# Kernel optimization log

Measured on AMD Instinct MI355X. Metric: run time of the kernel, lower is better.

## Reference

```python
import jax, jax.numpy as jnp
import numpy as np

BN = 128  # weight block rows
BK = 128  # quantization block along K
FP8_MAX = 448.0  # float8_e4m3fn max finite value
F8 = jnp.float8_e4m3fn


def _quant_dequant_act(x):
    # Dynamic per-token, per-128-block FP8 quantization (scale = amax/448), then dequant.
    M, K = x.shape
    xb = x.reshape(M, K // BK, BK)
    amax = jnp.max(jnp.abs(xb), axis=-1, keepdims=True)
    scale = jnp.maximum(amax, 1e-12) / FP8_MAX
    q = jnp.clip(xb / scale, -FP8_MAX, FP8_MAX).astype(F8)
    return (q.astype(jnp.float32) * scale).reshape(M, K)


def _dequant_weight(w, s):
    # w: (N, K) fp8, s: (N//BN, K//BK) f32 block scales
    N, K = w.shape
    sf = jnp.repeat(jnp.repeat(s, BN, axis=0), BK, axis=1)[:N, :K]
    return w.astype(jnp.float32) * sf


def _fp8_linear(x, w, s):
    # y = dequant(quant(x)) @ dequant(w)^T  -- matches w8a8_fp8_matmul semantics
    return _quant_dequant_act(x) @ _dequant_weight(w, s).T


def _quantize_weight(key, shape):
    E, N, K = shape
    w = jax.random.normal(key, shape, jnp.float32) * 0.02
    wb = w.reshape(E, N // BN, BN, K // BK, BK)
    amax = jnp.max(jnp.abs(wb), axis=(2, 4), keepdims=True)
    scale = jnp.maximum(amax, 1e-12) / FP8_MAX
    q = jnp.clip(wb / scale, -FP8_MAX, FP8_MAX).astype(F8).reshape(E, N, K)
    return q, scale.reshape(E, N // BN, K // BK)


def setup_inputs() -> dict:
    key = jax.random.key(0)
    k1, k2, k3, k4, k5 = jax.random.split(key, 5)
    T, H, I, E, TOPK = 2048, 2048, 1408, 8, 2
    hidden_states = jax.random.normal(k1, (T, H), jnp.float32)
    top_k_index = jax.random.randint(k2, (T, TOPK), 0, E).astype(jnp.int64)
    w = jax.random.uniform(k3, (T, TOPK), jnp.float32)
    top_k_weights = w / jnp.sum(w, axis=-1, keepdims=True)
    gate_up_proj, gate_up_proj_scale_inv = _quantize_weight(k4, (E, 2 * I, H))
    down_proj, down_proj_scale_inv = _quantize_weight(k5, (E, H, I))
    return {
        "hidden_states": hidden_states,
        "top_k_index": top_k_index,
        "top_k_weights": top_k_weights,
        "gate_up_proj": gate_up_proj,
        "gate_up_proj_scale_inv": gate_up_proj_scale_inv,
        "down_proj": down_proj,
        "down_proj_scale_inv": down_proj_scale_inv,
    }


def reference(hidden_states, top_k_index, top_k_weights, gate_up_proj,
              gate_up_proj_scale_inv, down_proj, down_proj_scale_inv):
    E = gate_up_proj.shape[0]
    I = down_proj.shape[-1]
    # Activation quantization is per-token: identical for every expert, compute once.
    x_dq = _quant_dequant_act(hidden_states)  # (T, H)
    out = jnp.zeros_like(hidden_states, dtype=jnp.float32)
    for e in range(E):  # fixed small expert loop (structural, not data dim)
        gu = x_dq @ _dequant_weight(gate_up_proj[e], gate_up_proj_scale_inv[e]).T  # (T, 2I)
        gate, up = gu[:, :I], gu[:, I:]
        h = jax.nn.silu(gate) * up
        d = _fp8_linear(h, down_proj[e], down_proj_scale_inv[e])  # (T, H)
        # routing weight for this expert per token (sums duplicates like index_add_)
        rw = jnp.sum(jnp.where(top_k_index == e, top_k_weights, 0.0), axis=-1)  # (T,)
        out = out + rw[:, None] * d
    return out.astype(hidden_states.dtype)
```

## Files before the change

kernel.cpp:

```cpp
#include <hip/hip_runtime.h>
#include <cstdint>
#include <cstddef>

using f32x4 = __attribute__((ext_vector_type(4))) float;

#define TDIM 2048
#define HDIM 2048
#define IDIM 1408
#define NEXP 8
#define NKB1 16
#define NNB1 11
#define NKB2 11
#define MAXM 4096

__device__ __forceinline__ void gll16(const void* g, void* l) {
  __builtin_amdgcn_global_load_lds(
      (__attribute__((address_space(1))) void*)(uintptr_t)g,
      (__attribute__((address_space(3))) void*)(uint32_t)(uintptr_t)l,
      16, 0, 0);
}

__device__ __forceinline__ f32x4 mfma_fp8(long a, long b, f32x4 c) {
  return __builtin_amdgcn_mfma_f32_16x16x32_fp8_fp8(a, b, c, 0, 0, 0);
}

__device__ __forceinline__ uint32_t f8_1(float q) {
  q = fminf(fmaxf(q, -448.f), 448.f);
  return (uint32_t)__builtin_amdgcn_cvt_pk_fp8_f32(q, q, 0, false) & 0xffu;
}

__device__ __forceinline__ float bf16_to_f32(uint32_t bits16) {
  union { uint32_t u; float f; } c;
  c.u = bits16 << 16;
  return c.f;
}

__global__ void sniff_kernel(const uint16_t* __restrict__ a,
                             const uint16_t* __restrict__ b,
                             int* __restrict__ modes, int* __restrict__ cnt) {
  if (threadIdx.x < 8) cnt[threadIdx.x] = 0;
  if (threadIdx.x == 0) {
    unsigned acc = 0;
    for (int i = 0; i < 128; ++i) acc |= a[2 * i];
    modes[0] = (acc == 0) ? 1 : 0;
    acc = 0;
    for (int i = 0; i < 128; ++i) acc |= b[2 * i];
    modes[1] = (acc == 0) ? 1 : 0;
  }
}

__global__ void repack_kernel(const void* __restrict__ in, uint8_t* __restrict__ out,
                              int n8, const int* __restrict__ modes, int midx) {
  const int i = blockIdx.x * 256 + threadIdx.x;
  if (i >= n8) return;
  const int m = modes[midx];
  float f[8];
  if (m == 1) {
    const float4* p = (const float4*)in;
    float4 a = p[2 * i], b = p[2 * i + 1];
    f[0] = a.x; f[1] = a.y; f[2] = a.z; f[3] = a.w;
    f[4] = b.x; f[5] = b.y; f[6] = b.z; f[7] = b.w;
  } else {
    uint4 v = ((const uint4*)in)[i];
#pragma unroll
    for (int j = 0; j < 4; ++j) {
      uint32_t w = (&v.x)[j];
      f[2 * j]     = bf16_to_f32(w & 0xffffu);
      f[2 * j + 1] = bf16_to_f32(w >> 16);
    }
  }
  uint32_t lo = 0, hi = 0;
#pragma unroll
  for (int j = 0; j < 8; ++j) {
    uint32_t b8 = f8_1(f[j]);
    if (j < 4) lo |= b8 << (8 * j);
    else       hi |= b8 << (8 * (j - 4));
  }
  ((uint2*)out)[i] = make_uint2(lo, hi);
}

__global__ void quantx_kernel(const float* __restrict__ x,
                              uint8_t* __restrict__ xq, float* __restrict__ xs) {
  const int gid = blockIdx.x * 4 + (threadIdx.x >> 6);
  const int lane = threadIdx.x & 63;
  const int r = gid >> 4, kb = gid & 15;
  const float2 v = *(const float2*)(x + (size_t)r * HDIM + kb * 128 + lane * 2);
  float a = fmaxf(fabsf(v.x), fabsf(v.y));
#pragma unroll
  for (int d = 1; d < 64; d <<= 1) a = fmaxf(a, __shfl_xor(a, d));
  const float s = fmaxf(a, 1e-12f) / 448.f;
  const uint32_t b0 = f8_1(v.x / s);
  const uint32_t b1 = f8_1(v.y / s);
  *(uint16_t*)(xq + (size_t)r * HDIM + kb * 128 + lane * 2) = (uint16_t)(b0 | (b1 << 8));
  if (lane == 0) xs[r * 16 + kb] = s;
}

__global__ void route_kernel(const void* __restrict__ idxraw,
                             int* __restrict__ list, int* __restrict__ cnt) {
  const long long* p = (const long long*)idxraw;
  unsigned hi = 0;
#pragma unroll
  for (int j = 0; j < 16; ++j) hi |= (unsigned)((unsigned long long)p[j] >> 32);
  const int i = blockIdx.x * 256 + threadIdx.x;
  int e;
  if (hi == 0) {
    e = (int)p[i];
  } else {
    long long v = p[i >> 1];
    e = (int)((i & 1) ? (v >> 32) : (v & 0xffffffffLL));
  }
  e &= 7;
  const int pos = atomicAdd(&cnt[e], 1);
  list[e * MAXM + pos] = i;
}

__global__ __launch_bounds__(256) void gemm1_kernel(
    const uint8_t* __restrict__ xq, const float* __restrict__ xs,
    const uint8_t* __restrict__ w, const float* __restrict__ wscl,
    const int* __restrict__ list, const int* __restrict__ cnt,
    uint8_t* __restrict__ hq, float* __restrict__ hs) {
  const int e = blockIdx.z, mt = blockIdx.y, nb = blockIdx.x;
  const int M = cnt[e];
  if (mt * 64 >= M) return;
  __shared__ __align__(16) uint8_t As[8192];
  __shared__ __align__(16) uint8_t Bg[16384];
  __shared__ __align__(16) uint8_t Bu[16384];
  __shared__ int slots[64];
  __shared__ __align__(16) float sxs[64];
  __shared__ __align__(16) float amx[128];
  const int tid = threadIdx.x, lane = tid & 63, wid = tid >> 6;
  const int wr = wid >> 1, wc = wid & 1;
  if (tid < 64) {
    int m = mt * 64 + tid;
    slots[tid] = list[e * MAXM + (m < M ? m : 0)];
  }
  __syncthreads();
  const int s = tid >> 3;
  const int cj0 = ((tid & 7) ^ (s & 7)) << 4;
  const long tokA0 = slots[s] >> 1;
  const long tokA1 = slots[s + 32] >> 1;
  const int my_tok = (tid < 64) ? (slots[tid] >> 1) : 0;
  const uint8_t* pA0 = xq + tokA0 * HDIM + cj0;
  const uint8_t* pA1 = xq + tokA1 * HDIM + cj0;
  const size_t wb = (size_t)e * (2 * IDIM) * HDIM;
  const uint8_t* pG = w + wb + (size_t)(nb * 128 + s) * HDIM + cj0;
  const uint8_t* pU = w + wb + (size_t)(IDIM + nb * 128 + s) * HDIM + cj0;
  const float* wsg = wscl + (size_t)e * 352 + nb * 16;
  const float* wsu = wsg + 176;
  const float* pSX = xs + (size_t)my_tok * 16;
  f32x4 accg[2][4] = {};
  f32x4 accu[2][4] = {};
  const int kbyte = (lane >> 4) << 3;
  float rs = (tid < 64) ? pSX[0] : 0.f;
  for (int kb = 0; kb < NKB1; ++kb) {
    __syncthreads();
    const int ko = kb << 7;
    gll16(pA0 + ko, As + tid * 16);
    gll16(pA1 + ko, As + 4096 + tid * 16);
#pragma unroll
    for (int k = 0; k < 4; ++k) {
      gll16(pG + (size_t)(k * 32) * HDIM + ko, Bg + k * 4096 + tid * 16);
      gll16(pU + (size_t)(k * 32) * HDIM + ko, Bu + k * 4096 + tid * 16);
    }
    if (tid < 64) sxs[tid] = rs;
    __syncthreads();
    if (kb + 1 < NKB1) rs = (tid < 64) ? pSX[kb + 1] : 0.f;
    const float swg = wsg[kb];
    const float swu = wsu[kb];
    long af[2][4], bgf[4][4], buf_[4][4];
#pragma unroll
    for (int mi = 0; mi < 2; ++mi) {
      const int r = wr * 32 + mi * 16 + (lane & 15);
      const int xr = (r & 7) << 4;
      const uint8_t* bp = As + r * 128;
#pragma unroll
      for (int kc = 0; kc < 4; ++kc)
        af[mi][kc] = *(const long*)(bp + (((kc << 5) + kbyte) ^ xr));
    }
#pragma unroll
    for (int ni = 0; ni < 4; ++ni) {
      const int r = wc * 64 + ni * 16 + (lane & 15);
      const int xr = (r & 7) << 4;
      const uint8_t* bpg = Bg + r * 128;
      const uint8_t* bpu = Bu + r * 128;
#pragma unroll
      for (int kc = 0; kc < 4; ++kc) {
        bgf[ni][kc] = *(const long*)(bpg + (((kc << 5) + kbyte) ^ xr));
        buf_[ni][kc] = *(const long*)(bpu + (((kc << 5) + kbyte) ^ xr));
      }
    }
    f32x4 sx[2];
#pragma unroll
    for (int mi = 0; mi < 2; ++mi)
      sx[mi] = *(const f32x4*)(sxs + wr * 32 + mi * 16 + ((lane >> 4) << 2));
#pragma unroll
    for (int mi = 0; mi < 2; ++mi)
#pragma unroll
      for (int ni = 0; ni < 4; ++ni) {
        f32x4 pg = {0.f, 0.f, 0.f, 0.f};
        f32x4 pu = {0.f, 0.f, 0.f, 0.f};
#pragma unroll
        for (int kc = 0; kc < 4; ++kc) {
          pg = mfma_fp8(af[mi][kc], bgf[ni][kc], pg);
          pu = mfma_fp8(af[mi][kc], buf_[ni][kc], pu);
        }
#pragma unroll
        for (int j = 0; j < 4; ++j) {
          accg[mi][ni][j] += pg[j] * (sx[mi][j] * swg);
          accu[mi][ni][j] += pu[j] * (sx[mi][j] * swu);
        }
      }
  }
  f32x4 hv[2][4];
  f32x4 rmax[2];
#pragma unroll
  for (int mi = 0; mi < 2; ++mi) {
#pragma unroll
    for (int ni = 0; ni < 4; ++ni)
#pragma unroll
      for (int j = 0; j < 4; ++j) {
        float g = accg[mi][ni][j];
        float u = accu[mi][ni][j];
        float h = (g / (1.f + expf(-g))) * u;
        hv[mi][ni][j] = h;
        float ah = fabsf(h);
        rmax[mi][j] = (ni == 0) ? ah : fmaxf(rmax[mi][j], ah);
      }
#pragma unroll
    for (int d = 1; d < 16; d <<= 1)
#pragma unroll
      for (int j = 0; j < 4; ++j)
        rmax[mi][j] = fmaxf(rmax[mi][j], __shfl_xor(rmax[mi][j], d));
  }
  __syncthreads();
  if ((lane & 15) == 0) {
#pragma unroll
    for (int mi = 0; mi < 2; ++mi)
#pragma unroll
      for (int j = 0; j < 4; ++j) {
        int row = wr * 32 + mi * 16 + ((lane >> 4) << 2) + j;
        amx[row * 2 + wc] = rmax[mi][j];
      }
  }
  __syncthreads();
  const int Mrem = M - mt * 64;
#pragma unroll
  for (int mi = 0; mi < 2; ++mi)
#pragma unroll
    for (int j = 0; j < 4; ++j) {
      const int row = wr * 32 + mi * 16 + ((lane >> 4) << 2) + j;
      float am = fmaxf(amx[row * 2], amx[row * 2 + 1]);
      float sq = fmaxf(am, 1e-12f) / 448.f;
      if (row < Mrem) {
        const int slot = slots[row];
        uint8_t* hp = hq + (size_t)slot * IDIM + nb * 128 + wc * 64 + (lane & 15);
#pragma unroll
        for (int ni = 0; ni < 4; ++ni)
          hp[ni * 16] = (uint8_t)f8_1(hv[mi][ni][j] / sq);
        if (wc == 0 && (lane & 15) == 0) hs[slot * 16 + nb] = sq;
      }
    }
}

__global__ __launch_bounds__(256) void gemm2_kernel(
    const uint8_t* __restrict__ hq, const float* __restrict__ hs,
    const uint8_t* __restrict__ w, const float* __restrict__ wscl,
    const int* __restrict__ list, const int* __restrict__ cnt,
    const float* __restrict__ tkw, float* __restrict__ tmp) {
  const int e = blockIdx.z, mt = blockIdx.y, nt = blockIdx.x;
  const int M = cnt[e];
  if (mt * 128 >= M) return;
  __shared__ __align__(16) uint8_t As[16384];
  __shared__ __align__(16) uint8_t Bs[16384];
  __shared__ int slots[128];
  __shared__ float rwl[128];
  __shared__ __align__(16) float sxs[128];
  const int tid = threadIdx.x, lane = tid & 63, wid = tid >> 6;
  const int wr = wid >> 1, wc = wid & 1;
  if (tid < 128) {
    int m = mt * 128 + tid;
    int slot = list[e * MAXM + (m < M ? m : 0)];
    slots[tid] = slot;
    rwl[tid] = (m < M) ? tkw[slot] : 0.f;
  }
  __syncthreads();
  const int s = tid >> 3;
  const int cj0 = ((tid & 7) ^ (s & 7)) << 4;
  const long sA0 = slots[s];
  const long sA1 = slots[s + 32];
  const long sA2 = slots[s + 64];
  const long sA3 = slots[s + 96];
  const int my_slot = (tid < 128) ? slots[tid] : 0;
  const uint8_t* pA0 = hq + sA0 * IDIM + cj0;
  const uint8_t* pA1 = hq + sA1 * IDIM + cj0;
  const uint8_t* pA2 = hq + sA2 * IDIM + cj0;
  const uint8_t* pA3 = hq + sA3 * IDIM + cj0;
  const uint8_t* pB = w + (size_t)e * HDIM * IDIM + (size_t)(nt * 128 + s) * IDIM + cj0;
  const float* wsd = wscl + (size_t)e * 176 + (nt + (wc >> 31)) * 11;
  const float* pSX = hs + (size_t)my_slot * 16;
  f32x4 acc[4][4] = {};
  const int kbyte = (lane >> 4) << 3;
  float rs = (tid < 128) ? pSX[0] : 0.f;
  for (int kb = 0; kb < NKB2; ++kb) {
    __syncthreads();
    const int ko = kb << 7;
    gll16(pA0 + ko, As + tid * 16);
    gll16(pA1 + ko, As + 4096 + tid * 16);
    gll16(pA2 + ko, As + 8192 + tid * 16);
    gll16(pA3 + ko, As + 12288 + tid * 16);
#pragma unroll
    for (int k = 0; k < 4; ++k)
      gll16(pB + (size_t)(k * 32) * IDIM + ko, Bs + k * 4096 + tid * 16);
    if (tid < 128) sxs[tid] = rs;
    __syncthreads();
    if (kb + 1 < NKB2) rs = (tid < 128) ? pSX[kb + 1] : 0.f;
    const float swd = wsd[kb];
    long af[4][4], bf[4][4];
#pragma unroll
    for (int mi = 0; mi < 4; ++mi) {
      const int r = wr * 64 + mi * 16 + (lane & 15);
      const int xr = (r & 7) << 4;
      const uint8_t* bp = As + r * 128;
#pragma unroll
      for (int kc = 0; kc < 4; ++kc)
        af[mi][kc] = *(const long*)(bp + (((kc << 5) + kbyte) ^ xr));
    }
#pragma unroll
    for (int ni = 0; ni < 4; ++ni) {
      const int r = wc * 64 + ni * 16 + (lane & 15);
      const int xr = (r & 7) << 4;
      const uint8_t* bp = Bs + r * 128;
#pragma unroll
      for (int kc = 0; kc < 4; ++kc)
        bf[ni][kc] = *(const long*)(bp + (((kc << 5) + kbyte) ^ xr));
    }
    f32x4 sx[4];
#pragma unroll
    for (int mi = 0; mi < 4; ++mi)
      sx[mi] = *(const f32x4*)(sxs + wr * 64 + mi * 16 + ((lane >> 4) << 2));
#pragma unroll
    for (int mi = 0; mi < 4; ++mi)
#pragma unroll
      for (int ni = 0; ni < 4; ++ni) {
        f32x4 p = {0.f, 0.f, 0.f, 0.f};
#pragma unroll
        for (int kc = 0; kc < 4; ++kc) p = mfma_fp8(af[mi][kc], bf[ni][kc], p);
#pragma unroll
        for (int j = 0; j < 4; ++j) acc[mi][ni][j] += p[j] * (sx[mi][j] * swd);
      }
  }
  const int Mrem = M - mt * 128;
#pragma unroll
  for (int mi = 0; mi < 4; ++mi)
#pragma unroll
    for (int j = 0; j < 4; ++j) {
      const int row = wr * 64 + mi * 16 + ((lane >> 4) << 2) + j;
      if (row < Mrem) {
        const int slot = slots[row];
        const float rw = rwl[row];
        float* op = tmp + (size_t)slot * HDIM + nt * 128 + wc * 64 + (lane & 15);
#pragma unroll
        for (int ni = 0; ni < 4; ++ni) op[ni * 16] = rw * acc[mi][ni][j];
      }
    }
}

__global__ void reduce_kernel(const float* __restrict__ tmp, float* __restrict__ out) {
  const int i = blockIdx.x * 256 + threadIdx.x;
  const int t = i >> 9, c4 = i & 511;
  const f32x4 a = ((const f32x4*)tmp)[(size_t)(2 * t) * 512 + c4];
  const f32x4 c = ((const f32x4*)tmp)[(size_t)(2 * t) * 512 + 512 + c4];
  ((f32x4*)out)[i] = a + c;
}

extern "C" void kernel_launch(void* const* d_in, const int* in_sizes, int n_in,
                              void* d_out, int out_size, void* d_ws, size_t ws_size,
                              hipStream_t stream) {
  const float* hidden = (const float*)d_in[0];
  const void* topk_idx = d_in[1];
  const float* topk_w = (const float*)d_in[2];
  const void* gup_raw = d_in[3];
  const float* gup_s = (const float*)d_in[4];
  const void* dwn_raw = d_in[5];
  const float* dwn_s = (const float*)d_in[6];
  float* out = (float*)d_out;
  uint8_t* ws = (uint8_t*)d_ws;
  uint8_t* xq = ws;
  float* xs = (float*)(ws + 4194304);
  uint8_t* hq = ws + 4325376;
  float* hs = (float*)(ws + 10092544);
  int* list = (int*)(ws + 10354688);
  int* cnt = (int*)(ws + 10485760);
  int* modes = (int*)(ws + 10485824);
  uint8_t* gq = ws + 10485888;
  float* tmp = (float*)gq;
  uint8_t* dq = ws + 56623232;
  (void)in_sizes; (void)n_in; (void)ws_size; (void)out_size;

  sniff_kernel<<<1, 64, 0, stream>>>((const uint16_t*)gup_raw, (const uint16_t*)dwn_raw, modes, cnt);
  repack_kernel<<<(5767168 + 255) / 256, 256, 0, stream>>>(gup_raw, gq, 5767168, modes, 0);
  repack_kernel<<<(2883584 + 255) / 256, 256, 0, stream>>>(dwn_raw, dq, 2883584, modes, 1);
  quantx_kernel<<<8192, 256, 0, stream>>>(hidden, xq, xs);
  route_kernel<<<16, 256, 0, stream>>>(topk_idx, list, cnt);
  gemm1_kernel<<<dim3(11, 64, 8), 256, 0, stream>>>(xq, xs, gq, gup_s, list, cnt, hq, hs);
  gemm2_kernel<<<dim3(16, 32, 8), 256, 0, stream>>>(hq, hs, dq, dwn_s, list, cnt, topk_w, tmp);
  reduce_kernel<<<4096, 256, 0, stream>>>(tmp, out);
}
```

Before: 241.5 us.

## Double-buffer LDS with 64-byte K steps and preload activation scales in both GEMMs

Both expert GEMM kernels now load K in 64-byte chunks into two LDS buffers, prefetching the next chunk with global_load_lds while MFMAs run on the current one. Each iteration ends with an explicit vmcnt wait and one barrier instead of two. All per-row activation scales are loaded into shared memory once before the loop rather than per iteration, and the LDS layout uses a new two-rows-per-line swizzle. This trades more loop iterations and barriers for overlap of memory traffic with compute, and the scale multiply is still applied every 64-byte step.

```diff
diff --git a/kernel.cpp b/kernel.cpp
--- a/kernel.cpp
+++ b/kernel.cpp
@@ -8,9 +8,8 @@
 #define HDIM 2048
 #define IDIM 1408
 #define NEXP 8
-#define NKB1 16
-#define NNB1 11
-#define NKB2 11
+#define NK1 32
+#define NK2 22
 #define MAXM 4096
 
 __device__ __forceinline__ void gll16(const void* g, void* l) {
@@ -33,6 +32,11 @@
   union { uint32_t u; float f; } c;
   c.u = bits16 << 16;
   return c.f;
+}
+
+__device__ __forceinline__ int lds_off(int r, int b) {
+  const int line = r >> 1;
+  return line * 128 + ((((r >> 3) ^ r) & 1) << 6) + ((((b >> 4) ^ line) & 3) << 4) + (b & 15);
 }
 
 __global__ void sniff_kernel(const uint16_t* __restrict__ a,
@@ -122,11 +126,11 @@
   const int e = blockIdx.z, mt = blockIdx.y, nb = blockIdx.x;
   const int M = cnt[e];
   if (mt * 64 >= M) return;
-  __shared__ __align__(16) uint8_t As[8192];
-  __shared__ __align__(16) uint8_t Bg[16384];
-  __shared__ __align__(16) uint8_t Bu[16384];
+  __shared__ __align__(16) uint8_t As[2 * 4096];
+  __shared__ __align__(16) uint8_t Bg[2 * 8192];
+  __shared__ __align__(16) uint8_t Bu[2 * 8192];
   __shared__ int slots[64];
-  __shared__ __align__(16) float sxs[64];
+  __shared__ __align__(16) float sxsAll[16][64];
   __shared__ __align__(16) float amx[128];
   const int tid = threadIdx.x, lane = tid & 63, wid = tid >> 6;
   const int wr = wid >> 1, wc = wid & 1;
@@ -135,64 +139,73 @@
     slots[tid] = list[e * MAXM + (m < M ? m : 0)];
   }
   __syncthreads();
-  const int s = tid >> 3;
-  const int cj0 = ((tid & 7) ^ (s & 7)) << 4;
-  const long tokA0 = slots[s] >> 1;
-  const long tokA1 = slots[s + 32] >> 1;
-  const int my_tok = (tid < 64) ? (slots[tid] >> 1) : 0;
-  const uint8_t* pA0 = xq + tokA0 * HDIM + cj0;
-  const uint8_t* pA1 = xq + tokA1 * HDIM + cj0;
+  if (tid < 64) {
+    const int tok = slots[tid] >> 1;
+    const f32x4* ps = (const f32x4*)(xs + (size_t)tok * 16);
+#pragma unroll
+    for (int q = 0; q < 4; ++q) {
+      f32x4 v = ps[q];
+      sxsAll[q * 4 + 0][tid] = v[0];
+      sxsAll[q * 4 + 1][tid] = v[1];
+      sxsAll[q * 4 + 2][tid] = v[2];
+      sxsAll[q * 4 + 3][tid] = v[3];
+    }
+  }
+  const int line = tid >> 3;
+  const int r0 = 2 * line + (((tid >> 2) & 1) ^ ((line >> 2) & 1));
+  const int srcch = ((tid & 3) ^ (line & 3)) << 4;
+  const long tokA = slots[r0] >> 1;
+  const uint8_t* pA = xq + tokA * HDIM + srcch;
   const size_t wb = (size_t)e * (2 * IDIM) * HDIM;
-  const uint8_t* pG = w + wb + (size_t)(nb * 128 + s) * HDIM + cj0;
-  const uint8_t* pU = w + wb + (size_t)(IDIM + nb * 128 + s) * HDIM + cj0;
+  const uint8_t* pG = w + wb + (size_t)(nb * 128 + r0) * HDIM + srcch;
+  const uint8_t* pU = w + wb + (size_t)(IDIM + nb * 128 + r0) * HDIM + srcch;
   const float* wsg = wscl + (size_t)e * 352 + nb * 16;
   const float* wsu = wsg + 176;
-  const float* pSX = xs + (size_t)my_tok * 16;
   f32x4 accg[2][4] = {};
   f32x4 accu[2][4] = {};
   const int kbyte = (lane >> 4) << 3;
-  float rs = (tid < 64) ? pSX[0] : 0.f;
-  for (int kb = 0; kb < NKB1; ++kb) {
-    __syncthreads();
-    const int ko = kb << 7;
-    gll16(pA0 + ko, As + tid * 16);
-    gll16(pA1 + ko, As + 4096 + tid * 16);
-#pragma unroll
-    for (int k = 0; k < 4; ++k) {
-      gll16(pG + (size_t)(k * 32) * HDIM + ko, Bg + k * 4096 + tid * 16);
-      gll16(pU + (size_t)(k * 32) * HDIM + ko, Bu + k * 4096 + tid * 16);
-    }
-    if (tid < 64) sxs[tid] = rs;
-    __syncthreads();
-    if (kb + 1 < NKB1) rs = (tid < 64) ? pSX[kb + 1] : 0.f;
-    const float swg = wsg[kb];
-    const float swu = wsu[kb];
-    long af[2][4], bgf[4][4], buf_[4][4];
+#define STAGE1(d, kk) { const int ko_ = (kk) << 6; \
+    gll16(pA + ko_, As + (d) * 4096 + tid * 16); \
+    gll16(pG + ko_, Bg + (d) * 8192 + tid * 16); \
+    gll16(pG + (size_t)64 * HDIM + ko_, Bg + (d) * 8192 + 4096 + tid * 16); \
+    gll16(pU + ko_, Bu + (d) * 8192 + tid * 16); \
+    gll16(pU + (size_t)64 * HDIM + ko_, Bu + (d) * 8192 + 4096 + tid * 16); }
+  STAGE1(0, 0)
+  __syncthreads();
+  int cur = 0;
+  for (int kb = 0; kb < NK1; ++kb) {
+    if (kb + 1 < NK1) STAGE1(cur ^ 1, kb + 1)
+    const float swg = wsg[kb >> 1];
+    const float swu = wsu[kb >> 1];
+    const uint8_t* Ab = As + cur * 4096;
+    const uint8_t* Bgb = Bg + cur * 8192;
+    const uint8_t* Bub = Bu + cur * 8192;
+    long af[2][2], bgf[4][2], buf_[4][2];
 #pragma unroll
     for (int mi = 0; mi < 2; ++mi) {
       const int r = wr * 32 + mi * 16 + (lane & 15);
-      const int xr = (r & 7) << 4;
-      const uint8_t* bp = As + r * 128;
-#pragma unroll
-      for (int kc = 0; kc < 4; ++kc)
-        af[mi][kc] = *(const long*)(bp + (((kc << 5) + kbyte) ^ xr));
+#pragma unroll
+      for (int kc = 0; kc < 2; ++kc)
+        af[mi][kc] = *(const long*)(Ab + lds_off(r, (kc << 5) + kbyte));
     }
 #pragma unroll
     for (int ni = 0; ni < 4; ++ni) {
       const int r = wc * 64 + ni * 16 + (lane & 15);
-      const int xr = (r & 7) << 4;
-      const uint8_t* bpg = Bg + r * 128;
-      const uint8_t* bpu = Bu + r * 128;
-#pragma unroll
-      for (int kc = 0; kc < 4; ++kc) {
-        bgf[ni][kc] = *(const long*)(bpg + (((kc << 5) + kbyte) ^ xr));
-        buf_[ni][kc] = *(const long*)(bpu + (((kc << 5) + kbyte) ^ xr));
-      }
-    }
-    f32x4 sx[2];
-#pragma unroll
-    for (int mi = 0; mi < 2; ++mi)
-      sx[mi] = *(const f32x4*)(sxs + wr * 32 + mi * 16 + ((lane >> 4) << 2));
+#pragma unroll
+      for (int kc = 0; kc < 2; ++kc) {
+        bgf[ni][kc] = *(const long*)(Bgb + lds_off(r, (kc << 5) + kbyte));
+        buf_[ni][kc] = *(const long*)(Bub + lds_off(r, (kc << 5) + kbyte));
+      }
+    }
+    f32x4 sxg[2], sxu[2];
+#pragma unroll
+    for (int mi = 0; mi < 2; ++mi) {
+      f32x4 sx = *(const f32x4*)(&sxsAll[kb >> 1][wr * 32 + mi * 16 + ((lane >> 4) << 2)]);
+      sxg[mi] = sx * swg;
+      sxu[mi] = sx * swu;
+    }
+    asm volatile("s_waitcnt lgkmcnt(0)" ::: "memory");
+    __builtin_amdgcn_sched_barrier(0);
 #pragma unroll
     for (int mi = 0; mi < 2; ++mi)
 #pragma unroll
@@ -200,17 +213,21 @@
         f32x4 pg = {0.f, 0.f, 0.f, 0.f};
         f32x4 pu = {0.f, 0.f, 0.f, 0.f};
 #pragma unroll
-        for (int kc = 0; kc < 4; ++kc) {
+        for (int kc = 0; kc < 2; ++kc) {
           pg = mfma_fp8(af[mi][kc], bgf[ni][kc], pg);
           pu = mfma_fp8(af[mi][kc], buf_[ni][kc], pu);
         }
 #pragma unroll
         for (int j = 0; j < 4; ++j) {
-          accg[mi][ni][j] += pg[j] * (sx[mi][j] * swg);
-          accu[mi][ni][j] += pu[j] * (sx[mi][j] * swu);
+          accg[mi][ni][j] += pg[j] * sxg[mi][j];
+          accu[mi][ni][j] += pu[j] * sxu[mi][j];
         }
       }
-  }
+    asm volatile("s_waitcnt vmcnt(0)" ::: "memory");
+    __builtin_amdgcn_s_barrier();
+    cur ^= 1;
+  }
+#undef STAGE1
   f32x4 hv[2][4];
   f32x4 rmax[2];
 #pragma unroll
@@ -270,11 +287,11 @@
   const int e = blockIdx.z, mt = blockIdx.y, nt = blockIdx.x;
   const int M = cnt[e];
   if (mt * 128 >= M) return;
-  __shared__ __align__(16) uint8_t As[16384];
-  __shared__ __align__(16) uint8_t Bs[16384];
+  __shared__ __align__(16) uint8_t As[2 * 8192];
+  __shared__ __align__(16) uint8_t Bs[2 * 8192];
   __shared__ int slots[128];
   __shared__ float rwl[128];
-  __shared__ __align__(16) float sxs[128];
+  __shared__ __align__(16) float sxsAll[16][128];
   const int tid = threadIdx.x, lane = tid & 63, wid = tid >> 6;
   const int wr = wid >> 1, wc = wid & 1;
   if (tid < 128) {
@@ -284,71 +301,80 @@
     rwl[tid] = (m < M) ? tkw[slot] : 0.f;
   }
   __syncthreads();
-  const int s = tid >> 3;
-  const int cj0 = ((tid & 7) ^ (s & 7)) << 4;
-  const long sA0 = slots[s];
-  const long sA1 = slots[s + 32];
-  const long sA2 = slots[s + 64];
-  const long sA3 = slots[s + 96];
-  const int my_slot = (tid < 128) ? slots[tid] : 0;
-  const uint8_t* pA0 = hq + sA0 * IDIM + cj0;
-  const uint8_t* pA1 = hq + sA1 * IDIM + cj0;
-  const uint8_t* pA2 = hq + sA2 * IDIM + cj0;
-  const uint8_t* pA3 = hq + sA3 * IDIM + cj0;
-  const uint8_t* pB = w + (size_t)e * HDIM * IDIM + (size_t)(nt * 128 + s) * IDIM + cj0;
-  const float* wsd = wscl + (size_t)e * 176 + (nt + (wc >> 31)) * 11;
-  const float* pSX = hs + (size_t)my_slot * 16;
+  if (tid < 128) {
+    const int slot = slots[tid];
+    const f32x4* ps = (const f32x4*)(hs + (size_t)slot * 16);
+#pragma unroll
+    for (int q = 0; q < 4; ++q) {
+      f32x4 v = ps[q];
+      sxsAll[q * 4 + 0][tid] = v[0];
+      sxsAll[q * 4 + 1][tid] = v[1];
+      sxsAll[q * 4 + 2][tid] = v[2];
+      sxsAll[q * 4 + 3][tid] = v[3];
+    }
+  }
+  const int line = tid >> 3;
+  const int r0 = 2 * line + (((tid >> 2) & 1) ^ ((line >> 2) & 1));
+  const int srcch = ((tid & 3) ^ (line & 3)) << 4;
+  const long sA0 = slots[r0];
+  const long sA1 = slots[r0 + 64];
+  const uint8_t* pA0 = hq + sA0 * IDIM + srcch;
+  const uint8_t* pA1 = hq + sA1 * IDIM + srcch;
+  const uint8_t* pB = w + (size_t)e * HDIM * IDIM + (size_t)(nt * 128 + r0) * IDIM + srcch;
+  const float* wsd = wscl + (size_t)e * 176 + nt * 11;
   f32x4 acc[4][4] = {};
   const int kbyte = (lane >> 4) << 3;
-  float rs = (tid < 128) ? pSX[0] : 0.f;
-  for (int kb = 0; kb < NKB2; ++kb) {
-    __syncthreads();
-    const int ko = kb << 7;
-    gll16(pA0 + ko, As + tid * 16);
-    gll16(pA1 + ko, As + 4096 + tid * 16);
-    gll16(pA2 + ko, As + 8192 + tid * 16);
-    gll16(pA3 + ko, As + 12288 + tid * 16);
-#pragma unroll
-    for (int k = 0; k < 4; ++k)
-      gll16(pB + (size_t)(k * 32) * IDIM + ko, Bs + k * 4096 + tid * 16);
-    if (tid < 128) sxs[tid] = rs;
-    __syncthreads();
-    if (kb + 1 < NKB2) rs = (tid < 128) ? pSX[kb + 1] : 0.f;
-    const float swd = wsd[kb];
-    long af[4][4], bf[4][4];
+#define STAGE2(d, kk) { const int ko_ = (kk) << 6; \
+    gll16(pA0 + ko_, As + (d) * 8192 + tid * 16); \
+    gll16(pA1 + ko_, As + (d) * 8192 + 4096 + tid * 16); \
+    gll16(pB + ko_, Bs + (d) * 8192 + tid * 16); \
+    gll16(pB + (size_t)64 * IDIM + ko_, Bs + (d) * 8192 + 4096 + tid * 16); }
+  STAGE2(0, 0)
+  __syncthreads();
+  int cur = 0;
+  for (int kb = 0; kb < NK2; ++kb) {
+    if (kb + 1 < NK2) STAGE2(cur ^ 1, kb + 1)
+    const float swd = wsd[kb >> 1];
+    const uint8_t* Ab = As + cur * 8192;
+    const uint8_t* Bb = Bs + cur * 8192;
+    long af[4][2], bf[4][2];
 #pragma unroll
     for (int mi = 0; mi < 4; ++mi) {
       const int r = wr * 64 + mi * 16 + (lane & 15);
-      const int xr = (r & 7) << 4;
-      const uint8_t* bp = As + r * 128;
-#pragma unroll
-      for (int kc = 0; kc < 4; ++kc)
-        af[mi][kc] = *(const long*)(bp + (((kc << 5) + kbyte) ^ xr));
+#pragma unroll
+      for (int kc = 0; kc < 2; ++kc)
+        af[mi][kc] = *(const long*)(Ab + lds_off(r, (kc << 5) + kbyte));
     }
 #pragma unroll
     for (int ni = 0; ni < 4; ++ni) {
       const int r = wc * 64 + ni * 16 + (lane & 15);
-      const int xr = (r & 7) << 4;
-      const uint8_t* bp = Bs + r * 128;
-#pragma unroll
-      for (int kc = 0; kc < 4; ++kc)
-        bf[ni][kc] = *(const long*)(bp + (((kc << 5) + kbyte) ^ xr));
-    }
-    f32x4 sx[4];
-#pragma unroll
-    for (int mi = 0; mi < 4; ++mi)
-      sx[mi] = *(const f32x4*)(sxs + wr * 64 + mi * 16 + ((lane >> 4) << 2));
+#pragma unroll
+      for (int kc = 0; kc < 2; ++kc)
+        bf[ni][kc] = *(const long*)(Bb + lds_off(r, (kc << 5) + kbyte));
+    }
+    f32x4 sxd[4];
+#pragma unroll
+    for (int mi = 0; mi < 4; ++mi) {
+      f32x4 sx = *(const f32x4*)(&sxsAll[kb >> 1][wr * 64 + mi * 16 + ((lane >> 4) << 2)]);
+      sxd[mi] = sx * swd;
+    }
+    asm volatile("s_waitcnt lgkmcnt(0)" ::: "memory");
+    __builtin_amdgcn_sched_barrier(0);
 #pragma unroll
     for (int mi = 0; mi < 4; ++mi)
 #pragma unroll
       for (int ni = 0; ni < 4; ++ni) {
         f32x4 p = {0.f, 0.f, 0.f, 0.f};
 #pragma unroll
-        for (int kc = 0; kc < 4; ++kc) p = mfma_fp8(af[mi][kc], bf[ni][kc], p);
-#pragma unroll
-        for (int j = 0; j < 4; ++j) acc[mi][ni][j] += p[j] * (sx[mi][j] * swd);
-      }
-  }
+        for (int kc = 0; kc < 2; ++kc) p = mfma_fp8(af[mi][kc], bf[ni][kc], p);
+#pragma unroll
+        for (int j = 0; j < 4; ++j) acc[mi][ni][j] += p[j] * sxd[mi][j];
+      }
+    asm volatile("s_waitcnt vmcnt(0)" ::: "memory");
+    __builtin_amdgcn_s_barrier();
+    cur ^= 1;
+  }
+#undef STAGE2
   const int Mrem = M - mt * 128;
 #pragma unroll
   for (int mi = 0; mi < 4; ++mi)
```

Measured after the change: 249.8 us. +3.4%, slower.

## Use 512-thread blocks with 2x4 wave grid; shrink gemm2 M tile to 64

Applied to the files above, without the earlier changes.

Both grouped GEMM kernels move from 256 to 512 threads, laid out as 2x4 waves, so each wave owns a 32x32 output sub-tile instead of 32x64 or 64x64. gemm2 halves its M tile from 128 to 64 rows and doubles the grid in y, which gives more blocks per expert and less padding waste. The per-row activation scale times the weight scale is now computed once per k-block instead of inside the inner loop. The intent is more waves for latency hiding and better load balance, at the cost of less register-level reuse per wave and more B-tile reloads in gemm2.

```diff
diff --git a/kernel.cpp b/kernel.cpp
--- a/kernel.cpp
+++ b/kernel.cpp
@@ -9,7 +9,6 @@
 #define IDIM 1408
 #define NEXP 8
 #define NKB1 16
-#define NNB1 11
 #define NKB2 11
 #define MAXM 4096
 
@@ -114,7 +113,7 @@
   list[e * MAXM + pos] = i;
 }
 
-__global__ __launch_bounds__(256) void gemm1_kernel(
+__global__ __launch_bounds__(512) void gemm1_kernel(
     const uint8_t* __restrict__ xq, const float* __restrict__ xs,
     const uint8_t* __restrict__ w, const float* __restrict__ wscl,
     const int* __restrict__ list, const int* __restrict__ cnt,
@@ -127,47 +126,43 @@
   __shared__ __align__(16) uint8_t Bu[16384];
   __shared__ int slots[64];
   __shared__ __align__(16) float sxs[64];
-  __shared__ __align__(16) float amx[128];
+  __shared__ __align__(16) float amx[256];
   const int tid = threadIdx.x, lane = tid & 63, wid = tid >> 6;
-  const int wr = wid >> 1, wc = wid & 1;
+  const int wr = wid >> 2, wc = wid & 3;
   if (tid < 64) {
     int m = mt * 64 + tid;
     slots[tid] = list[e * MAXM + (m < M ? m : 0)];
   }
   __syncthreads();
-  const int s = tid >> 3;
-  const int cj0 = ((tid & 7) ^ (s & 7)) << 4;
-  const long tokA0 = slots[s] >> 1;
-  const long tokA1 = slots[s + 32] >> 1;
+  const int sr = tid >> 3;
+  const int cj0 = ((tid & 7) ^ (sr & 7)) << 4;
+  const long tokA = slots[sr] >> 1;
   const int my_tok = (tid < 64) ? (slots[tid] >> 1) : 0;
-  const uint8_t* pA0 = xq + tokA0 * HDIM + cj0;
-  const uint8_t* pA1 = xq + tokA1 * HDIM + cj0;
+  const uint8_t* pA = xq + tokA * HDIM + cj0;
   const size_t wb = (size_t)e * (2 * IDIM) * HDIM;
-  const uint8_t* pG = w + wb + (size_t)(nb * 128 + s) * HDIM + cj0;
-  const uint8_t* pU = w + wb + (size_t)(IDIM + nb * 128 + s) * HDIM + cj0;
+  const uint8_t* pG = w + wb + (size_t)(nb * 128 + sr) * HDIM + cj0;
+  const uint8_t* pU = w + wb + (size_t)(IDIM + nb * 128 + sr) * HDIM + cj0;
   const float* wsg = wscl + (size_t)e * 352 + nb * 16;
   const float* wsu = wsg + 176;
   const float* pSX = xs + (size_t)my_tok * 16;
-  f32x4 accg[2][4] = {};
-  f32x4 accu[2][4] = {};
+  f32x4 accg[2][2] = {};
+  f32x4 accu[2][2] = {};
   const int kbyte = (lane >> 4) << 3;
   float rs = (tid < 64) ? pSX[0] : 0.f;
   for (int kb = 0; kb < NKB1; ++kb) {
     __syncthreads();
     const int ko = kb << 7;
-    gll16(pA0 + ko, As + tid * 16);
-    gll16(pA1 + ko, As + 4096 + tid * 16);
-#pragma unroll
-    for (int k = 0; k < 4; ++k) {
-      gll16(pG + (size_t)(k * 32) * HDIM + ko, Bg + k * 4096 + tid * 16);
-      gll16(pU + (size_t)(k * 32) * HDIM + ko, Bu + k * 4096 + tid * 16);
-    }
+    gll16(pA + ko, As + tid * 16);
+    gll16(pG + ko, Bg + tid * 16);
+    gll16(pG + (size_t)64 * HDIM + ko, Bg + 8192 + tid * 16);
+    gll16(pU + ko, Bu + tid * 16);
+    gll16(pU + (size_t)64 * HDIM + ko, Bu + 8192 + tid * 16);
     if (tid < 64) sxs[tid] = rs;
     __syncthreads();
     if (kb + 1 < NKB1) rs = (tid < 64) ? pSX[kb + 1] : 0.f;
     const float swg = wsg[kb];
     const float swu = wsu[kb];
-    long af[2][4], bgf[4][4], buf_[4][4];
+    long af[2][4], bgf[2][4], buf_[2][4];
 #pragma unroll
     for (int mi = 0; mi < 2; ++mi) {
       const int r = wr * 32 + mi * 16 + (lane & 15);
@@ -178,8 +173,8 @@
         af[mi][kc] = *(const long*)(bp + (((kc << 5) + kbyte) ^ xr));
     }
 #pragma unroll
-    for (int ni = 0; ni < 4; ++ni) {
-      const int r = wc * 64 + ni * 16 + (lane & 15);
+    for (int ni = 0; ni < 2; ++ni) {
+      const int r = wc * 32 + ni * 16 + (lane & 15);
       const int xr = (r & 7) << 4;
       const uint8_t* bpg = Bg + r * 128;
       const uint8_t* bpu = Bu + r * 128;
@@ -189,14 +184,17 @@
         buf_[ni][kc] = *(const long*)(bpu + (((kc << 5) + kbyte) ^ xr));
       }
     }
-    f32x4 sx[2];
+    f32x4 sxg[2], sxu[2];
+#pragma unroll
+    for (int mi = 0; mi < 2; ++mi) {
+      f32x4 sx = *(const f32x4*)(sxs + wr * 32 + mi * 16 + ((lane >> 4) << 2));
+      sxg[mi] = sx * swg;
+      sxu[mi] = sx * swu;
+    }
 #pragma unroll
     for (int mi = 0; mi < 2; ++mi)
-      sx[mi] = *(const f32x4*)(sxs + wr * 32 + mi * 16 + ((lane >> 4) << 2));
-#pragma unroll
-    for (int mi = 0; mi < 2; ++mi)
-#pragma unroll
-      for (int ni = 0; ni < 4; ++ni) {
+#pragma unroll
+      for (int ni = 0; ni < 2; ++ni) {
         f32x4 pg = {0.f, 0.f, 0.f, 0.f};
         f32x4 pu = {0.f, 0.f, 0.f, 0.f};
 #pragma unroll
@@ -206,17 +204,17 @@
         }
 #pragma unroll
         for (int j = 0; j < 4; ++j) {
-          accg[mi][ni][j] += pg[j] * (sx[mi][j] * swg);
-          accu[mi][ni][j] += pu[j] * (sx[mi][j] * swu);
+          accg[mi][ni][j] += pg[j] * sxg[mi][j];
+          accu[mi][ni][j] += pu[j] * sxu[mi][j];
         }
       }
   }
-  f32x4 hv[2][4];
+  f32x4 hv[2][2];
   f32x4 rmax[2];
 #pragma unroll
   for (int mi = 0; mi < 2; ++mi) {
 #pragma unroll
-    for (int ni = 0; ni < 4; ++ni)
+    for (int ni = 0; ni < 2; ++ni)
 #pragma unroll
       for (int j = 0; j < 4; ++j) {
         float g = accg[mi][ni][j];
@@ -239,7 +237,7 @@
 #pragma unroll
       for (int j = 0; j < 4; ++j) {
         int row = wr * 32 + mi * 16 + ((lane >> 4) << 2) + j;
-        amx[row * 2 + wc] = rmax[mi][j];
+        amx[row * 4 + wc] = rmax[mi][j];
       }
   }
   __syncthreads();
@@ -249,76 +247,66 @@
 #pragma unroll
     for (int j = 0; j < 4; ++j) {
       const int row = wr * 32 + mi * 16 + ((lane >> 4) << 2) + j;
-      float am = fmaxf(amx[row * 2], amx[row * 2 + 1]);
+      f32x4 a4 = *(const f32x4*)(amx + row * 4);
+      float am = fmaxf(fmaxf(a4[0], a4[1]), fmaxf(a4[2], a4[3]));
       float sq = fmaxf(am, 1e-12f) / 448.f;
       if (row < Mrem) {
         const int slot = slots[row];
-        uint8_t* hp = hq + (size_t)slot * IDIM + nb * 128 + wc * 64 + (lane & 15);
-#pragma unroll
-        for (int ni = 0; ni < 4; ++ni)
-          hp[ni * 16] = (uint8_t)f8_1(hv[mi][ni][j] / sq);
+        uint8_t* hp = hq + (size_t)slot * IDIM + nb * 128 + wc * 32 + (lane & 15);
+        hp[0]  = (uint8_t)f8_1(hv[mi][0][j] / sq);
+        hp[16] = (uint8_t)f8_1(hv[mi][1][j] / sq);
         if (wc == 0 && (lane & 15) == 0) hs[slot * 16 + nb] = sq;
       }
     }
 }
 
-__global__ __launch_bounds__(256) void gemm2_kernel(
+__global__ __launch_bounds__(512) void gemm2_kernel(
     const uint8_t* __restrict__ hq, const float* __restrict__ hs,
     const uint8_t* __restrict__ w, const float* __restrict__ wscl,
     const int* __restrict__ list, const int* __restrict__ cnt,
     const float* __restrict__ tkw, float* __restrict__ tmp) {
   const int e = blockIdx.z, mt = blockIdx.y, nt = blockIdx.x;
   const int M = cnt[e];
-  if (mt * 128 >= M) return;
-  __shared__ __align__(16) uint8_t As[16384];
+  if (mt * 64 >= M) return;
+  __shared__ __align__(16) uint8_t As[8192];
   __shared__ __align__(16) uint8_t Bs[16384];
-  __shared__ int slots[128];
-  __shared__ float rwl[128];
-  __shared__ __align__(16) float sxs[128];
+  __shared__ int slots[64];
+  __shared__ float rwl[64];
+  __shared__ __align__(16) float sxs[64];
   const int tid = threadIdx.x, lane = tid & 63, wid = tid >> 6;
-  const int wr = wid >> 1, wc = wid & 1;
-  if (tid < 128) {
-    int m = mt * 128 + tid;
+  const int wr = wid >> 2, wc = wid & 3;
+  if (tid < 64) {
+    int m = mt * 64 + tid;
     int slot = list[e * MAXM + (m < M ? m : 0)];
     slots[tid] = slot;
     rwl[tid] = (m < M) ? tkw[slot] : 0.f;
   }
   __syncthreads();
-  const int s = tid >> 3;
-  const int cj0 = ((tid & 7) ^ (s & 7)) << 4;
-  const long sA0 = slots[s];
-  const long sA1 = slots[s + 32];
-  const long sA2 = slots[s + 64];
-  const long sA3 = slots[s + 96];
-  const int my_slot = (tid < 128) ? slots[tid] : 0;
-  const uint8_t* pA0 = hq + sA0 * IDIM + cj0;
-  const uint8_t* pA1 = hq + sA1 * IDIM + cj0;
-  const uint8_t* pA2 = hq + sA2 * IDIM + cj0;
-  const uint8_t* pA3 = hq + sA3 * IDIM + cj0;
-  const uint8_t* pB = w + (size_t)e * HDIM * IDIM + (size_t)(nt * 128 + s) * IDIM + cj0;
-  const float* wsd = wscl + (size_t)e * 176 + (nt + (wc >> 31)) * 11;
+  const int sr = tid >> 3;
+  const int cj0 = ((tid & 7) ^ (sr & 7)) << 4;
+  const long sA = slots[sr];
+  const int my_slot = (tid < 64) ? slots[tid] : 0;
+  const uint8_t* pA = hq + sA * IDIM + cj0;
+  const uint8_t* pB = w + (size_t)e * HDIM * IDIM + (size_t)(nt * 128 + sr) * IDIM + cj0;
+  const float* wsd = wscl + (size_t)e * 176 + nt * 11;
   const float* pSX = hs + (size_t)my_slot * 16;
-  f32x4 acc[4][4] = {};
+  f32x4 acc[2][2] = {};
   const int kbyte = (lane >> 4) << 3;
-  float rs = (tid < 128) ? pSX[0] : 0.f;
+  float rs = (tid < 64) ? pSX[0] : 0.f;
   for (int kb = 0; kb < NKB2; ++kb) {
     __syncthreads();
     const int ko = kb << 7;
-    gll16(pA0 + ko, As + tid * 16);
-    gll16(pA1 + ko, As + 4096 + tid * 16);
-    gll16(pA2 + ko, As + 8192 + tid * 16);
-    gll16(pA3 + ko, As + 12288 + tid * 16);
-#pragma unroll
-    for (int k = 0; k < 4; ++k)
-      gll16(pB + (size_t)(k * 32) * IDIM + ko, Bs + k * 4096 + tid * 16);
-    if (tid < 128) sxs[tid] = rs;
+    gll16(pA + ko, As + tid * 16);
+    gll16(pB + ko, Bs + tid * 16);
+    gll16(pB + (size_t)64 * IDIM + ko, Bs + 8192 + tid * 16);
+    if (tid < 64) sxs[tid] = rs;
     __syncthreads();
-    if (kb + 1 < NKB2) rs = (tid < 128) ? pSX[kb + 1] : 0.f;
+    if (kb + 1 < NKB2) rs = (tid < 64) ? pSX[kb + 1] : 0.f;
     const float swd = wsd[kb];
-    long af[4][4], bf[4][4];
-#pragma unroll
-    for (int mi = 0; mi < 4; ++mi) {
-      const int r = wr * 64 + mi * 16 + (lane & 15);
+    long af[2][4], bf[2][4];
+#pragma unroll
+    for (int mi = 0; mi < 2; ++mi) {
+      const int r = wr * 32 + mi * 16 + (lane & 15);
       const int xr = (r & 7) << 4;
       const uint8_t* bp = As + r * 128;
 #pragma unroll
@@ -326,41 +314,43 @@
         af[mi][kc] = *(const long*)(bp + (((kc << 5) + kbyte) ^ xr));
     }
 #pragma unroll
-    for (int ni = 0; ni < 4; ++ni) {
-      const int r = wc * 64 + ni * 16 + (lane & 15);
+    for (int ni = 0; ni < 2; ++ni) {
+      const int r = wc * 32 + ni * 16 + (lane & 15);
       const int xr = (r & 7) << 4;
       const uint8_t* bp = Bs + r * 128;
 #pragma unroll
       for (int kc = 0; kc < 4; ++kc)
         bf[ni][kc] = *(const long*)(bp + (((kc << 5) + kbyte) ^ xr));
     }
-    f32x4 sx[4];
-#pragma unroll
-    for (int mi = 0; mi < 4; ++mi)
-      sx[mi] = *(const f32x4*)(sxs + wr * 64 + mi * 16 + ((lane >> 4) << 2));
-#pragma unroll
-    for (int mi = 0; mi < 4; ++mi)
-#pragma unroll
-      for (int ni = 0; ni < 4; ++ni) {
+    f32x4 sxd[2];
+#pragma unroll
+    for (int mi = 0; mi < 2; ++mi) {
+      f32x4 sx = *(const f32x4*)(sxs + wr * 32 + mi * 16 + ((lane >> 4) << 2));
+      sxd[mi] = sx * swd;
+    }
+#pragma unroll
+    for (int mi = 0; mi < 2; ++mi)
+#pragma unroll
+      for (int ni = 0; ni < 2; ++ni) {
         f32x4 p = {0.f, 0.f, 0.f, 0.f};
 #pragma unroll
         for (int kc = 0; kc < 4; ++kc) p = mfma_fp8(af[mi][kc], bf[ni][kc], p);
 #pragma unroll
-        for (int j = 0; j < 4; ++j) acc[mi][ni][j] += p[j] * (sx[mi][j] * swd);
-      }
-  }
-  const int Mrem = M - mt * 128;
-#pragma unroll
-  for (int mi = 0; mi < 4; ++mi)
+        for (int j = 0; j < 4; ++j) acc[mi][ni][j] += p[j] * sxd[mi][j];
+      }
+  }
+  const int Mrem = M - mt * 64;
+#pragma unroll
+  for (int mi = 0; mi < 2; ++mi)
 #pragma unroll
     for (int j = 0; j < 4; ++j) {
-      const int row = wr * 64 + mi * 16 + ((lane >> 4) << 2) + j;
+      const int row = wr * 32 + mi * 16 + ((lane >> 4) << 2) + j;
       if (row < Mrem) {
         const int slot = slots[row];
         const float rw = rwl[row];
-        float* op = tmp + (size_t)slot * HDIM + nt * 128 + wc * 64 + (lane & 15);
-#pragma unroll
-        for (int ni = 0; ni < 4; ++ni) op[ni * 16] = rw * acc[mi][ni][j];
+        float* op = tmp + (size_t)slot * HDIM + nt * 128 + wc * 32 + (lane & 15);
+        op[0]  = rw * acc[mi][0][j];
+        op[16] = rw * acc[mi][1][j];
       }
     }
 }
@@ -402,7 +392,7 @@
   repack_kernel<<<(2883584 + 255) / 256, 256, 0, stream>>>(dwn_raw, dq, 2883584, modes, 1);
   quantx_kernel<<<8192, 256, 0, stream>>>(hidden, xq, xs);
   route_kernel<<<16, 256, 0, stream>>>(topk_idx, list, cnt);
-  gemm1_kernel<<<dim3(11, 64, 8), 256, 0, stream>>>(xq, xs, gq, gup_s, list, cnt, hq, hs);
-  gemm2_kernel<<<dim3(16, 32, 8), 256, 0, stream>>>(hq, hs, dq, dwn_s, list, cnt, topk_w, tmp);
+  gemm1_kernel<<<dim3(11, 64, 8), 512, 0, stream>>>(xq, xs, gq, gup_s, list, cnt, hq, hs);
+  gemm2_kernel<<<dim3(16, 64, 8), 512, 0, stream>>>(hq, hs, dq, dwn_s, list, cnt, topk_w, tmp);
   reduce_kernel<<<4096, 256, 0, stream>>>(tmp, out);
 }
```

New measurement: 317.5 us. 31.5% more time.
